# Performance work log

Hardware: AMD Instinct MI355X
Metric: run time of the kernel (lower is better)

## Reference

```python
import jax, jax.numpy as jnp
import numpy as np
from jax import lax


def setup_inputs() -> dict:
    key = jax.random.key(0)
    k1, k2, k3 = jax.random.split(key, 3)
    B, C, H, W = 32, 256, 64, 64
    x = jax.random.normal(k1, (B, C, H, W), dtype=jnp.float32)
    # ECA conv1d: 1 in-ch, 1 out-ch, kernel 5 (derived from C=256), no bias
    conv1d_w = jax.random.normal(k2, (1, 1, 5), dtype=jnp.float32) * 0.3
    # Spatial conv2d: 2 in-ch, 1 out-ch, kernel 7, with bias
    conv2d_w = jax.random.normal(k3, (1, 2, 7, 7), dtype=jnp.float32) * 0.1
    conv2d_b = jnp.zeros((1,), dtype=jnp.float32)
    return {"x": x, "conv1d_w": conv1d_w, "conv2d_w": conv2d_w, "conv2d_b": conv2d_b}


def reference(x, conv1d_w, conv2d_w, conv2d_b):
    # --- ECA channel attention ---
    # global avg pool over H,W -> [B, C]
    y = jnp.mean(x, axis=(2, 3))
    # conv1d across the channel axis (treated as length), 1 feature channel
    y = y[:, None, :]  # [B, 1, C]
    y = lax.conv_general_dilated(
        y, conv1d_w, window_strides=(1,), padding=[(2, 2)],
        dimension_numbers=("NCH", "OIH", "NCH"))
    ch_w = jax.nn.sigmoid(y)[:, 0, :, None, None]  # [B, C, 1, 1]
    eca_out = x * ch_w

    # --- spatial attention ---
    max_pool = jnp.max(x, axis=1, keepdims=True)   # [B,1,H,W]
    avg_pool = jnp.mean(x, axis=1, keepdims=True)  # [B,1,H,W]
    sp_in = jnp.concatenate([max_pool, avg_pool], axis=1)  # [B,2,H,W]
    sp = lax.conv_general_dilated(
        sp_in, conv2d_w, window_strides=(1, 1), padding=[(3, 3), (3, 3)],
        dimension_numbers=("NCHW", "OIHW", "NCHW"))
    sp = jax.nn.sigmoid(sp + conv2d_b[None, :, None, None])  # [B,1,H,W]

    return eca_out + x * sp + x
```

## Files before the change

### kernel.cpp

```cpp
#include <hip/hip_runtime.h>
#include <math.h>

#define BB 32
#define CC 256
#define HH 64
#define WW 64
#define HWSZ (HH * WW)
#define NCHUNK 16

__global__ __launch_bounds__(256, 2) void stats_kernel(
    const float* __restrict__ x, float* __restrict__ chan_part,
    float* __restrict__ pool_max, float* __restrict__ pool_sum) {
  const int b = blockIdx.x >> 4;
  const int chunk = blockIdx.x & 15;
  const int hw0 = chunk << 8;
  const int tid = threadIdx.x;
  const int wave = tid >> 6;
  const int lane = tid & 63;
  const int c_base = wave << 6;

  const float4* xp =
      (const float4*)(x + ((size_t)b << 20) + ((size_t)c_base << 12) + hw0) + lane;

  float4 mx = make_float4(-3.4e38f, -3.4e38f, -3.4e38f, -3.4e38f);
  float4 sm = make_float4(0.f, 0.f, 0.f, 0.f);

  for (int g = 0; g < 4; ++g) {
    float s[16];
#pragma unroll
    for (int ci = 0; ci < 16; ++ci) {
      const float4 v = xp[(g * 16 + ci) * (HWSZ / 4)];
      mx.x = fmaxf(mx.x, v.x); mx.y = fmaxf(mx.y, v.y);
      mx.z = fmaxf(mx.z, v.z); mx.w = fmaxf(mx.w, v.w);
      sm.x += v.x; sm.y += v.y; sm.z += v.z; sm.w += v.w;
      s[ci] = (v.x + v.y) + (v.z + v.w);
    }
#pragma unroll
    for (int ci = 0; ci < 16; ++ci) {
      float v = s[ci];
#pragma unroll
      for (int off = 32; off > 0; off >>= 1) v += __shfl_xor(v, off, 64);
      s[ci] = v;
    }
    if (lane == 0) {
      float4* cp = (float4*)(chan_part +
                             ((size_t)(b * NCHUNK + chunk)) * CC + c_base + g * 16);
      cp[0] = make_float4(s[0],  s[1],  s[2],  s[3]);
      cp[1] = make_float4(s[4],  s[5],  s[6],  s[7]);
      cp[2] = make_float4(s[8],  s[9],  s[10], s[11]);
      cp[3] = make_float4(s[12], s[13], s[14], s[15]);
    }
  }

  __shared__ float4 lmax[4][64];
  __shared__ float4 lsum[4][64];
  lmax[wave][lane] = mx;
  lsum[wave][lane] = sm;
  __syncthreads();
  if (tid < 64) {
    const float4 a = lmax[0][tid], b4 = lmax[1][tid];
    const float4 c4 = lmax[2][tid], d4 = lmax[3][tid];
    float4 M;
    M.x = fmaxf(fmaxf(a.x, b4.x), fmaxf(c4.x, d4.x));
    M.y = fmaxf(fmaxf(a.y, b4.y), fmaxf(c4.y, d4.y));
    M.z = fmaxf(fmaxf(a.z, b4.z), fmaxf(c4.z, d4.z));
    M.w = fmaxf(fmaxf(a.w, b4.w), fmaxf(c4.w, d4.w));
    const float4 sa = lsum[0][tid], sb = lsum[1][tid];
    const float4 sc = lsum[2][tid], sd = lsum[3][tid];
    float4 S;
    S.x = (sa.x + sb.x) + (sc.x + sd.x);
    S.y = (sa.y + sb.y) + (sc.y + sd.y);
    S.z = (sa.z + sb.z) + (sc.z + sd.z);
    S.w = (sa.w + sb.w) + (sc.w + sd.w);
    ((float4*)(pool_max + ((size_t)b << 12) + hw0))[tid] = M;
    ((float4*)(pool_sum + ((size_t)b << 12) + hw0))[tid] = S;
  }
}

__global__ __launch_bounds__(256) void eca_kernel(
    const float* __restrict__ chan_part, const float* __restrict__ w5,
    float* __restrict__ ch_w) {
  __shared__ float m[CC];
  const int b = blockIdx.x;
  const int c = threadIdx.x;
  float s = 0.0f;
#pragma unroll
  for (int k = 0; k < NCHUNK; ++k) s += chan_part[(size_t)(b * NCHUNK + k) * CC + c];
  m[c] = s * (1.0f / HWSZ);
  __syncthreads();

  float acc = 0.0f;
#pragma unroll
  for (int k = 0; k < 5; ++k) {
    int cc = c + k - 2;
    float v = (cc >= 0 && cc < CC) ? m[cc] : 0.0f;
    acc = fmaf(v, w5[k], acc);
  }
  ch_w[b * CC + c] = 1.0f / (1.0f + __expf(-acc));
}

__global__ __launch_bounds__(256) void spatial_kernel(
    const float* __restrict__ pool_max, const float* __restrict__ pool_sum,
    const float* __restrict__ w2, const float* __restrict__ bias,
    float* __restrict__ sp) {
  const int idx = blockIdx.x * 256 + threadIdx.x;
  const int b = idx >> 12;
  const int hw = idx & (HWSZ - 1);
  const int h = hw >> 6;
  const int w = hw & 63;

  float acc = bias[0];
#pragma unroll
  for (int kh = 0; kh < 7; ++kh) {
    const int hh = h + kh - 3;
    if (hh < 0 || hh >= HH) continue;
#pragma unroll
    for (int kw = 0; kw < 7; ++kw) {
      const int ww = w + kw - 3;
      if (ww < 0 || ww >= WW) continue;
      const int off = b * HWSZ + hh * WW + ww;
      acc = fmaf(pool_max[off], w2[kh * 7 + kw], acc);
      acc = fmaf(pool_sum[off], w2[49 + kh * 7 + kw] * (1.0f / CC), acc);
    }
  }
  sp[idx] = 1.0f / (1.0f + __expf(-acc));
}

__global__ __launch_bounds__(256) void combine_kernel(
    const float* __restrict__ x, const float* __restrict__ ch_w,
    const float* __restrict__ sp, float* __restrict__ out) {
  const size_t f = (size_t)blockIdx.x * 256 + threadIdx.x;
  const size_t e = f * 4;
  const int b = (int)(e >> 20);
  const int c = (int)(e >> 12) & 255;
  const int hw = (int)e & (HWSZ - 1);

  const float4 x4 = ((const float4*)x)[f];
  const float4 s4 = ((const float4*)(sp + ((size_t)b << 12)))[hw >> 2];
  const float cw = ch_w[b * CC + c] + 1.0f;

  float4 o;
  o.x = x4.x * (cw + s4.x);
  o.y = x4.y * (cw + s4.y);
  o.z = x4.z * (cw + s4.z);
  o.w = x4.w * (cw + s4.w);
  ((float4*)out)[f] = o;
}

extern "C" void kernel_launch(void* const* d_in, const int* in_sizes, int n_in,
                              void* d_out, int out_size, void* d_ws, size_t ws_size,
                              hipStream_t stream) {
  const float* x    = (const float*)d_in[0];
  const float* w1   = (const float*)d_in[1];
  const float* w2   = (const float*)d_in[2];
  const float* bias = (const float*)d_in[3];
  float* out = (float*)d_out;

  float* ws = (float*)d_ws;
  float* chan_part = ws;
  float* ch_w      = ws + 131072;
  float* pool_max  = ws + 139264;
  float* pool_sum  = ws + 270336;
  float* sp        = ws + 401408;

  stats_kernel<<<BB * NCHUNK, 256, 0, stream>>>(x, chan_part, pool_max, pool_sum);
  eca_kernel<<<BB, 256, 0, stream>>>(chan_part, w1, ch_w);
  spatial_kernel<<<(BB * HWSZ) / 256, 256, 0, stream>>>(pool_max, pool_sum, w2, bias, sp);
  combine_kernel<<<(BB * CC * HWSZ) / (4 * 256), 256, 0, stream>>>(x, ch_w, sp, out);
}
```

Before: 259.3 us.

## Fuse ECA, spatial conv and combine into one kernel per batch-chunk

Replaces the eca, spatial and combine kernels with one fused kernel launched per (batch, 256-pixel chunk). Each block recomputes the channel weights from the partial sums, loads a haloed 10x72 pooled tile into shared memory for the 7x7 conv, and then applies the combine over all 256 channels using nontemporal stores. This removes two launches and the global round trips for ch_w and sp. In exchange, every block redundantly recomputes the channel conv, only 512 blocks cover the 128M-element combine pass, and each thread walks 64 channels with strided loads.

```diff
diff --git a/kernel.cpp b/kernel.cpp
--- a/kernel.cpp
+++ b/kernel.cpp
@@ -7,6 +7,8 @@
 #define WW 64
 #define HWSZ (HH * WW)
 #define NCHUNK 16
+
+typedef float f32x4 __attribute__((ext_vector_type(4)));
 
 __global__ __launch_bounds__(256, 2) void stats_kernel(
     const float* __restrict__ x, float* __restrict__ chan_part,
@@ -77,74 +79,92 @@
   }
 }
 
-__global__ __launch_bounds__(256) void eca_kernel(
-    const float* __restrict__ chan_part, const float* __restrict__ w5,
-    float* __restrict__ ch_w) {
+__global__ __launch_bounds__(256) void fused_kernel(
+    const float* __restrict__ x, const float* __restrict__ chan_part,
+    const float* __restrict__ pool_max, const float* __restrict__ pool_sum,
+    const float* __restrict__ w5, const float* __restrict__ w2,
+    const float* __restrict__ bias, float* __restrict__ out) {
+  const int b = blockIdx.x >> 4;
+  const int chunk = blockIdx.x & 15;
+  const int hw0 = chunk << 8;
+  const int r0 = chunk << 2;
+  const int tid = threadIdx.x;
+  const int wave = tid >> 6;
+  const int lane4 = tid & 63;
+
   __shared__ float m[CC];
-  const int b = blockIdx.x;
-  const int c = threadIdx.x;
-  float s = 0.0f;
+  __shared__ float chw_s[CC];
+  __shared__ float tmax[10][72];
+  __shared__ float tsum[10][72];
+  __shared__ float sp_s[256];
+
+  {
+    float s = 0.0f;
 #pragma unroll
-  for (int k = 0; k < NCHUNK; ++k) s += chan_part[(size_t)(b * NCHUNK + k) * CC + c];
-  m[c] = s * (1.0f / HWSZ);
+    for (int k = 0; k < NCHUNK; ++k)
+      s += chan_part[(size_t)(b * NCHUNK + k) * CC + tid];
+    m[tid] = s * (1.0f / HWSZ);
+  }
+
+  for (int idx = tid; idx < 720; idx += 256) {
+    const int row = idx / 72;
+    const int col = idx - row * 72;
+    const int hh = r0 - 3 + row;
+    const int wcol = col - 3;
+    float vm = 0.0f, vs = 0.0f;
+    if (hh >= 0 && hh < HH && wcol >= 0 && wcol < WW) {
+      const int off = (b << 12) + (hh << 6) + wcol;
+      vm = pool_max[off];
+      vs = pool_sum[off];
+    }
+    tmax[row][col] = vm;
+    tsum[row][col] = vs;
+  }
   __syncthreads();
 
-  float acc = 0.0f;
+  {
+    float acc = 0.0f;
 #pragma unroll
-  for (int k = 0; k < 5; ++k) {
-    int cc = c + k - 2;
-    float v = (cc >= 0 && cc < CC) ? m[cc] : 0.0f;
-    acc = fmaf(v, w5[k], acc);
+    for (int k = 0; k < 5; ++k) {
+      const int cc = tid + k - 2;
+      const float v = (cc >= 0 && cc < CC) ? m[cc] : 0.0f;
+      acc = fmaf(v, w5[k], acc);
+    }
+    chw_s[tid] = 1.0f + 1.0f / (1.0f + __expf(-acc));
   }
-  ch_w[b * CC + c] = 1.0f / (1.0f + __expf(-acc));
-}
 
-__global__ __launch_bounds__(256) void spatial_kernel(
-    const float* __restrict__ pool_max, const float* __restrict__ pool_sum,
-    const float* __restrict__ w2, const float* __restrict__ bias,
-    float* __restrict__ sp) {
-  const int idx = blockIdx.x * 256 + threadIdx.x;
-  const int b = idx >> 12;
-  const int hw = idx & (HWSZ - 1);
-  const int h = hw >> 6;
-  const int w = hw & 63;
+  {
+    const int lr = tid >> 6;
+    const int w = tid & 63;
+    float acc = bias[0];
+#pragma unroll
+    for (int kh = 0; kh < 7; ++kh) {
+#pragma unroll
+      for (int kw = 0; kw < 7; ++kw) {
+        acc = fmaf(tmax[lr + kh][w + kw], w2[kh * 7 + kw], acc);
+        acc = fmaf(tsum[lr + kh][w + kw], w2[49 + kh * 7 + kw] * (1.0f / CC), acc);
+      }
+    }
+    sp_s[tid] = 1.0f / (1.0f + __expf(-acc));
+  }
+  __syncthreads();
 
-  float acc = bias[0];
-#pragma unroll
-  for (int kh = 0; kh < 7; ++kh) {
-    const int hh = h + kh - 3;
-    if (hh < 0 || hh >= HH) continue;
-#pragma unroll
-    for (int kw = 0; kw < 7; ++kw) {
-      const int ww = w + kw - 3;
-      if (ww < 0 || ww >= WW) continue;
-      const int off = b * HWSZ + hh * WW + ww;
-      acc = fmaf(pool_max[off], w2[kh * 7 + kw], acc);
-      acc = fmaf(pool_sum[off], w2[49 + kh * 7 + kw] * (1.0f / CC), acc);
-    }
+  const float4* xb = (const float4*)(x + ((size_t)b << 20) + hw0);
+  f32x4* ob = (f32x4*)(out + ((size_t)b << 20) + hw0);
+  const float4 sp4 = ((const float4*)sp_s)[lane4];
+
+#pragma unroll 4
+  for (int cg = 0; cg < 64; ++cg) {
+    const int c = (cg << 2) + wave;
+    const float cw = chw_s[c];
+    const float4 x4 = xb[(c << 10) + lane4];
+    f32x4 o;
+    o.x = x4.x * (cw + sp4.x);
+    o.y = x4.y * (cw + sp4.y);
+    o.z = x4.z * (cw + sp4.z);
+    o.w = x4.w * (cw + sp4.w);
+    __builtin_nontemporal_store(o, ob + (c << 10) + lane4);
   }
-  sp[idx] = 1.0f / (1.0f + __expf(-acc));
-}
-
-__global__ __launch_bounds__(256) void combine_kernel(
-    const float* __restrict__ x, const float* __restrict__ ch_w,
-    const float* __restrict__ sp, float* __restrict__ out) {
-  const size_t f = (size_t)blockIdx.x * 256 + threadIdx.x;
-  const size_t e = f * 4;
-  const int b = (int)(e >> 20);
-  const int c = (int)(e >> 12) & 255;
-  const int hw = (int)e & (HWSZ - 1);
-
-  const float4 x4 = ((const float4*)x)[f];
-  const float4 s4 = ((const float4*)(sp + ((size_t)b << 12)))[hw >> 2];
-  const float cw = ch_w[b * CC + c] + 1.0f;
-
-  float4 o;
-  o.x = x4.x * (cw + s4.x);
-  o.y = x4.y * (cw + s4.y);
-  o.z = x4.z * (cw + s4.z);
-  o.w = x4.w * (cw + s4.w);
-  ((float4*)out)[f] = o;
 }
 
 extern "C" void kernel_launch(void* const* d_in, const int* in_sizes, int n_in,
@@ -158,13 +178,10 @@
 
   float* ws = (float*)d_ws;
   float* chan_part = ws;
-  float* ch_w      = ws + 131072;
-  float* pool_max  = ws + 139264;
-  float* pool_sum  = ws + 270336;
-  float* sp        = ws + 401408;
+  float* pool_max  = ws + 131072;
+  float* pool_sum  = ws + 262144;
 
   stats_kernel<<<BB * NCHUNK, 256, 0, stream>>>(x, chan_part, pool_max, pool_sum);
-  eca_kernel<<<BB, 256, 0, stream>>>(chan_part, w1, ch_w);
-  spatial_kernel<<<(BB * HWSZ) / 256, 256, 0, stream>>>(pool_max, pool_sum, w2, bias, sp);
-  combine_kernel<<<(BB * CC * HWSZ) / (4 * 256), 256, 0, stream>>>(x, ch_w, sp, out);
+  fused_kernel<<<BB * NCHUNK, 256, 0, stream>>>(
+      x, chan_part, pool_max, pool_sum, w1, w2, bias, out);
 }
```

After: 267.9 us. 3.4% more time.
